# Kernel tuning notes

Hardware: AMD Instinct MI355X
Metric: run time of the kernel (lower is better)

The kernel has to match this reference:

```python
import jax, jax.numpy as jnp
from jax import lax
import numpy as np
import math

N_BLOCK = 10
CH = 64          # channels (nf)
IN_CH = 3        # input image channels
K = 3            # kernel size
COND_CH = 128    # conv_index='22' condition channel
B, H, W = 4, 128, 128


def setup_inputs() -> dict:
    key = jax.random.key(0)
    ks = jax.random.split(key, 8)
    x = jax.random.normal(ks[0], (B, IN_CH, H, W), jnp.float32)
    condition_feature = jax.random.normal(ks[1], (B, COND_CH, 1, 1), jnp.float32)
    # BaseConv2d params are torch.randn (initialize_weights skips BaseConv2d/EqualLinear)
    in_w = jax.random.normal(ks[2], (CH, IN_CH, K, K), jnp.float32)
    in_b = jnp.zeros((CH,), jnp.float32)
    blk_w = jax.random.normal(ks[3], (N_BLOCK, 2, CH, CH, K, K), jnp.float32)
    blk_b = jnp.zeros((N_BLOCK, 2, CH), jnp.float32)
    mod_w = jax.random.normal(ks[4], (N_BLOCK * 2, CH, COND_CH), jnp.float32)  # EqualLinear weights
    mod_b = jnp.ones((N_BLOCK * 2, CH), jnp.float32)                           # bias_init=1
    up_w = jax.random.normal(ks[5], (2, 4 * CH, CH, K, K), jnp.float32)        # two x2 pixel-shuffle stages
    up_b = jnp.zeros((2, 4 * CH), jnp.float32)
    out_w = jax.random.normal(ks[6], (IN_CH, CH, K, K), jnp.float32)
    out_b = jnp.zeros((IN_CH,), jnp.float32)
    return dict(x=x, condition_feature=condition_feature, in_w=in_w, in_b=in_b,
                blk_w=blk_w, blk_b=blk_b, mod_w=mod_w, mod_b=mod_b,
                up_w=up_w, up_b=up_b, out_w=out_w, out_b=out_b)


def _conv(x, w, b):
    out = lax.conv_general_dilated(x, w, (1, 1), [(K // 2, K // 2)] * 2,
                                   dimension_numbers=('NCHW', 'OIHW', 'NCHW'))
    return out + b[None, :, None, None]


def _mod_conv(x, w, bias, cond, scale):
    # x [b,c,h,w]; w [out,in,k,k]; cond [b,1,in,1,1] -> per-sample modulated weights
    wmod = w[None] * scale * cond  # [b,out,in,k,k]
    conv1 = lambda xi, wi: lax.conv_general_dilated(
        xi[None], wi, (1, 1), [(K // 2, K // 2)] * 2,
        dimension_numbers=('NCHW', 'OIHW', 'NCHW'))[0]
    out = jax.vmap(conv1)(x, wmod)  # groups=batch grouped conv
    # faithful to torch.repeat_interleave(bias, repeats=b) split across groups
    b_ = x.shape[0]
    bmat = jnp.repeat(bias, b_).reshape(b_, bias.shape[0])
    return out + bmat[:, :, None, None]


def _pixel_shuffle(x, r):
    b, c, h, w = x.shape
    C = c // (r * r)
    return x.reshape(b, C, r, r, h, w).transpose(0, 1, 4, 2, 5, 3).reshape(b, C, h * r, w * r)


def reference(x, condition_feature, in_w, in_b, blk_w, blk_b, mod_w, mod_b,
              up_w, up_b, out_w, out_b):
    b = x.shape[0]
    s_in = 1.0 / math.sqrt(IN_CH * K * K)
    s64 = 1.0 / math.sqrt(CH * K * K)
    s_lin = 1.0 / math.sqrt(COND_CH)

    # Modulations: 20 EqualLinears on [b,128] -> [10,2,b,1,64,1,1]
    cf = condition_feature.reshape(b, COND_CH)
    feats = jnp.einsum('bc,moc->mbo', cf, mod_w) * s_lin + mod_b[:, None, :]
    cond_feats = feats.reshape(N_BLOCK, 2, b, 1, CH, 1, 1)

    fea = _conv(x, in_w * s_in, in_b)
    for i in range(N_BLOCK):
        res = _mod_conv(fea, blk_w[i, 0], blk_b[i, 0], cond_feats[i, 0], s64)
        res = jax.nn.relu(res)
        res = _mod_conv(res, blk_w[i, 1], blk_b[i, 1], cond_feats[i, 1], s64)
        fea = res + fea  # residual_lr = 1
    for j in range(2):  # scale=4 -> two (conv, PixelShuffle(2)) stages
        fea = _conv(fea, up_w[j] * s64, up_b[j])
        fea = _pixel_shuffle(fea, 2)
    out = _conv(fea, out_w * s64, out_b)
    return out
```

## Files before the change

kernel.cpp:

```cpp
#include <hip/hip_runtime.h>
#include <math.h>

typedef unsigned short u16;
typedef unsigned int u32;
typedef float f32x4 __attribute__((ext_vector_type(4)));
typedef _Float16 f16;
typedef f16 f16x8 __attribute__((ext_vector_type(8)));
typedef f16 f16x4 __attribute__((ext_vector_type(4)));
typedef u32 u32x4 __attribute__((ext_vector_type(4)));


__device__ u16  g_bufT[(size_t)4*128*128*64];
__device__ float g_bufR[(size_t)4*128*128*64];
__device__ u16  g_bufB[(size_t)4*128*128*64];
__device__ u16  g_bufC[(size_t)4*4*256*256*16];
__device__ u16  g_bufE[(size_t)4*4*512*512*16];
__device__ float g_mod[20*4*64];
__device__ f16 g_wblk[(size_t)20*4*36864];
__device__ f16 g_wup[(size_t)2*4*36864];
__device__ f16 g_wout[9216];
__device__ u16 g_zero[8];

__device__ __forceinline__ void gll16(const void* g, void* l) {
    __builtin_amdgcn_global_load_lds(
        (const __attribute__((address_space(1))) unsigned*)g,
        (__attribute__((address_space(3))) unsigned*)l, 16, 0, 0);
}

__global__ void mod_kernel(const float* __restrict__ cf,
                           const float* __restrict__ mw,
                           const float* __restrict__ mb,
                           float* __restrict__ mod) {
    int m = blockIdx.x, b = blockIdx.y, o = threadIdx.x;
    const float* wrow = mw + (m * 64 + o) * 128;
    const float* cfb  = cf + b * 128;
    float s = 0.f;
#pragma unroll 8
    for (int c = 0; c < 128; ++c) s = fmaf(cfb[c], wrow[c], s);
    mod[(m * 4 + b) * 64 + o] = s * 0.08838834764831845f + mb[m * 64 + o];
}

__global__ void prep_blk_kernel(const float* __restrict__ bw,
                                const float* __restrict__ mod,
                                f16* __restrict__ wp) {
    int c = blockIdx.x, b = blockIdx.y;
    const float s64 = 1.0f / 24.0f;
    size_t base = (size_t)(c * 4 + b) * 36864;
    for (int idx = threadIdx.x; idx < 36864; idx += 256) {
        int j = idx & 7, l = (idx >> 3) & 63;
        int frag = idx >> 9;
        int mt = frag & 3, kfr = frag >> 2;
        int kf = kfr & 1, tap = kfr >> 1;
        int oc = mt * 16 + (l & 15);
        int ic = kf * 32 + (l >> 4) * 8 + j;
        float val = bw[((size_t)(c * 64 + oc) * 64 + ic) * 9 + tap] * s64 *
                    mod[(c * 4 + b) * 64 + ic];
        wp[base + idx] = (f16)val;
    }
}

__global__ void prep_up_kernel(const float* __restrict__ uw, f16* __restrict__ wp) {
    int st = blockIdx.x, ocg = blockIdx.y;
    const float s64 = 1.0f / 24.0f;
    size_t base = (size_t)(st * 4 + ocg) * 36864;
    for (int idx = threadIdx.x; idx < 36864; idx += 256) {
        int j = idx & 7, l = (idx >> 3) & 63;
        int frag = idx >> 9;
        int mt = frag & 3, kfr = frag >> 2;
        int kf = kfr & 1, tap = kfr >> 1;
        int oc = ocg * 64 + mt * 16 + (l & 15);
        int ic = kf * 32 + (l >> 4) * 8 + j;
        wp[base + idx] = (f16)(uw[((size_t)(st * 256 + oc) * 64 + ic) * 9 + tap] * s64);
    }
}

__global__ void prep_out_kernel(const float* __restrict__ ow, f16* __restrict__ wp) {
    const float s64 = 1.0f / 24.0f;
    for (int idx = threadIdx.x; idx < 9216; idx += 256) {
        int j = idx & 7, l = (idx >> 3) & 63;
        int frag = idx >> 9;
        int kf = frag & 1, tap = frag >> 1;
        int oc = l & 15;
        int ic = kf * 32 + (l >> 4) * 8 + j;
        float val = (oc < 3) ? ow[((size_t)(oc * 64) + ic) * 9 + tap] * s64 : 0.f;
        wp[idx] = (f16)val;
    }
}

__global__ __launch_bounds__(256) void in_conv_kernel(
    const float* __restrict__ in, const float* __restrict__ wgt,
    const float* __restrict__ bias, float* __restrict__ outR,
    u16* __restrict__ outT) {
    __shared__ float slds[3][34][35];
    __shared__ float wlds[3 * 9 * 16];
    const int H = 128, W = 128;
    const int tid = threadIdx.x, x = tid & 31, yb = tid >> 5;
    const int b = blockIdx.z >> 2, ocb = (blockIdx.z & 3) * 16;
    const int tY = blockIdx.y * 32, tX = blockIdx.x * 32;
    const float s_in = 0.19245008972987526f;

    float acc[16][4];
#pragma unroll
    for (int oc = 0; oc < 16; ++oc)
#pragma unroll
        for (int k = 0; k < 4; ++k) acc[oc][k] = 0.f;

    for (int idx = tid; idx < 3 * 34 * 34; idx += 256) {
        int ic = idx / (34 * 34), p = idx % (34 * 34);
        int r = p / 34, c = p % 34;
        int gy = tY + r - 1, gx = tX + c - 1;
        float v = 0.f;
        if (gy >= 0 && gy < H && gx >= 0 && gx < W)
            v = in[((b * 3 + ic) * H + gy) * W + gx] * s_in;
        slds[ic][r][c] = v;
    }
    for (int idx = tid; idx < 3 * 9 * 16; idx += 256) {
        int oc = idx & 15, tap = (idx >> 4) % 9, ic = idx / 144;
        wlds[idx] = wgt[((ocb + oc) * 3 + ic) * 9 + tap];
    }
    __syncthreads();

#pragma unroll
    for (int ic = 0; ic < 3; ++ic)
#pragma unroll
        for (int dy = 0; dy < 3; ++dy)
#pragma unroll
            for (int dx = 0; dx < 3; ++dx) {
                float xv[4];
#pragma unroll
                for (int k = 0; k < 4; ++k)
                    xv[k] = slds[ic][yb + 8 * k + dy][x + dx];
                const float* wrow = &wlds[(ic * 9 + dy * 3 + dx) * 16];
#pragma unroll
                for (int oc = 0; oc < 16; ++oc) {
                    float wv = wrow[oc];
#pragma unroll
                    for (int k = 0; k < 4; ++k) acc[oc][k] = fmaf(wv, xv[k], acc[oc][k]);
                }
            }

#pragma unroll
    for (int oc = 0; oc < 16; ++oc) {
        int goc = ocb + oc;
        float bv = bias[goc];
#pragma unroll
        for (int k = 0; k < 4; ++k) {
            int gy = tY + yb + 8 * k, gx = tX + x;
            size_t pixG = ((size_t)b * H + gy) * W + gx;
            float v = acc[oc][k] + bv;
            outR[pixG * 64 + goc] = v;
            outT[pixG * 64 + goc] = __builtin_bit_cast(u16, (f16)v);
        }
    }
}

template <int CG, int RG, int MG, int MT, int ROWS, int INMODE, int OUTMODE, int LB>
__global__ __launch_bounds__(256, LB) void mconv(
    const u16* __restrict__ inh, const f16* __restrict__ wp,
    const float* __restrict__ bias, float* __restrict__ rbuf,
    void* __restrict__ outv, u16* __restrict__ outT,
    int H, int W, int OCG, int wp_bstride, size_t in_pl, size_t out_pl)
{
    constexpr int TC = CG * 16, TR = RG * ROWS;
    constexpr int CST = TC + 2, RST = TR + 2;
    constexpr int PXT = RST * CST;
    constexpr int PXP = (PXT + 63) & ~63;
    constexpr int MT_W = MT / MG;
    constexpr int NW = CG * RG * MG;
    constexpr int SB_H = 4 * PXP * 8;
    constexpr int SA_H = 2 * 3 * MT * 512;

    __shared__ __align__(16) u16 smem[SB_H + SA_H];
    u16* sB = smem;
    u16* sA = smem + SB_H;

    const int tid = threadIdx.x;
    const int lane = tid & 63, wv = tid >> 6;
    const int lcol = lane & 15, lk8 = lane >> 4;
    const int cg = (CG > 1) ? (wv % CG) : 0;
    const int rg = (wv / CG) % RG;
    const int mg = wv / (CG * RG);
    const int b = blockIdx.z / OCG, ocg = blockIdx.z % OCG;
    const int y0 = blockIdx.y * TR, x0 = blockIdx.x * TC;
    const f16* wpb = wp + (size_t)b * wp_bstride + (size_t)ocg * 36864;

    auto stageA = [&](int kf, int dx, int buf) {
        for (int f = wv; f < 3 * MT; f += NW) {
            int dy = f / MT, mt = f - dy * MT;
            const f16* src = wpb + ((size_t)((dy * 3 + dx) * 2 + kf) * MT + mt) * 512 + lane * 8;
            gll16(src, sA + ((size_t)(buf * 3 * MT + f)) * 512 + lane * 8);
        }
    };
    auto stageB = [&](int kf) {
        for (int g0 = wv * 64; g0 < 4 * PXP; g0 += NW * 64) {
            int g = g0 + lane;
            int pl = g / PXP, px = g - pl * PXP;
            int t = px / CST, c = px - t * CST;
            int gy = y0 + t - 1, gx = x0 + c - 1;
            const void* src = g_zero;
            if (px < PXT && gy >= 0 && gy < H && gx >= 0 && gx < W) {
                size_t pix = ((size_t)b * H + gy) * W + gx;
                int ic = kf * 32 + pl * 8;
                if (INMODE == 1)
                    src = inh + pix * 64 + ic;
                else
                    src = inh + (size_t)(ic >> 4) * in_pl + pix * 16 + (ic & 15);
            }
            gll16(src, sB + (size_t)g * 8);
        }
    };

    f32x4 acc[ROWS][MT_W];
#pragma unroll
    for (int r = 0; r < ROWS; ++r)
#pragma unroll
        for (int m = 0; m < MT_W; ++m) acc[r][m] = (f32x4)0.f;

    stageB(0);
    stageA(0, 0, 0);
    __syncthreads();

    for (int s = 0; s < 6; ++s) {
        int kf = s / 3, dx = s - kf * 3;
        if (s == 3) {
            stageB(1);
            __syncthreads();
        }
        if (s < 5) {
            int ns = s + 1;
            stageA(ns / 3, ns % 3, ns & 1);
        }
        f16x8 Af[3][MT_W];
        const int abase = (s & 1) * 3 * MT;
#pragma unroll
        for (int dy = 0; dy < 3; ++dy)
#pragma unroll
            for (int m = 0; m < MT_W; ++m)
                Af[dy][m] = *(const f16x8*)(sA + (size_t)(abase + dy * MT + mg * MT_W + m) * 512 + lane * 8);

        const u16* bbase = sB + (size_t)lk8 * PXP * 8;
        const int pcol = cg * 16 + dx + lcol;
#pragma unroll
        for (int iy = 0; iy < ROWS + 2; ++iy) {
            int px = (rg * ROWS + iy) * CST + pcol;
            f16x8 Bf = *(const f16x8*)(bbase + (size_t)px * 8);
#pragma unroll
            for (int dy = 0; dy < 3; ++dy) {
                constexpr int unused = 0; (void)unused;
                int r = iy - dy;
                if (r >= 0 && r < ROWS) {
#pragma unroll
                    for (int m = 0; m < MT_W; ++m)
                        acc[r][m] = __builtin_amdgcn_mfma_f32_16x16x32_f16(
                            Af[dy][m], Bf, acc[r][m], 0, 0, 0);
                }
            }
        }
        __syncthreads();
    }

    if (OUTMODE == 0 || OUTMODE == 1) {
        u16* outh = (u16*)outv;
#pragma unroll
        for (int r = 0; r < ROWS; ++r) {
            int gy = y0 + rg * ROWS + r, gx = x0 + cg * 16 + lcol;
            size_t pixG = ((size_t)b * H + gy) * W + gx;
#pragma unroll
            for (int m = 0; m < MT_W; ++m) {
                int oc0 = (mg * MT_W + m) * 16 + lk8 * 4;
                f32x4 v = acc[r][m] + *(const f32x4*)(bias + oc0);
                if (OUTMODE == 0) {
                    f16x4 o;
#pragma unroll
                    for (int j = 0; j < 4; ++j) o[j] = (f16)fmaxf(v[j], 0.f);
                    *(f16x4*)(outh + pixG * 64 + oc0) = o;
                } else {
                    float* rp = rbuf + pixG * 64 + oc0;
                    f32x4 rv = *(const f32x4*)rp;
                    v += rv;
                    *(f32x4*)rp = v;
                    f16x4 o;
#pragma unroll
                    for (int j = 0; j < 4; ++j) o[j] = (f16)v[j];
                    *(f16x4*)(outT + pixG * 64 + oc0) = o;
                }
            }
        }
    } else if (OUTMODE == 2) {
        constexpr int NP = 2 * TR * TC;
        __syncthreads();
        u32* sT = (u32*)smem;
#pragma unroll
        for (int r = 0; r < ROWS; ++r) {
#pragma unroll
            for (int m = 0; m < MT_W; ++m) {
                int oc0 = m * 16 + lk8 * 4;
                int cc = m * 4 + lk8;
                f32x4 v = acc[r][m] + *(const f32x4*)(bias + ocg * 64 + oc0);
                int oy = 2 * (rg * ROWS + r);
#pragma unroll
                for (int jp = 0; jp < 2; ++jp) {
                    f16 e0 = (f16)v[jp * 2], e1 = (f16)v[jp * 2 + 1];
                    u32 w = (u32)__builtin_bit_cast(u16, e0) |
                            ((u32)__builtin_bit_cast(u16, e1) << 16);
                    sT[cc * NP + (oy + jp) * TC + cg * 16 + lcol] = w;
                }
            }
        }
        __syncthreads();
        u16* outh = (u16*)outv + (size_t)ocg * out_pl;
        const int H2 = 2 * H, W2 = 2 * W;
#pragma unroll
        for (int it = 0; it < NP / 256; ++it) {
            int p = tid + it * 256;
            int oy = p / TC, xp = p - oy * TC;
            u32 tv[16];
#pragma unroll
            for (int c = 0; c < 16; ++c) tv[c] = sT[c * NP + p];
            u32 q0[8], q1[8];
#pragma unroll
            for (int c2 = 0; c2 < 8; ++c2) {
                q0[c2] = (tv[2 * c2] & 0xffffu) | (tv[2 * c2 + 1] << 16);
                q1[c2] = (tv[2 * c2] >> 16) | (tv[2 * c2 + 1] & 0xffff0000u);
            }
            int gy2 = 2 * y0 + oy, gx2 = 2 * x0 + 2 * xp;
            u16* dst = outh + (((size_t)b * H2 + gy2) * W2 + gx2) * 16;
            *(u32x4*)(dst)      = *(u32x4*)(q0);
            *(u32x4*)(dst + 8)  = *(u32x4*)(q0 + 4);
            *(u32x4*)(dst + 16) = *(u32x4*)(q1);
            *(u32x4*)(dst + 24) = *(u32x4*)(q1 + 4);
        }
    } else {
        float* outp = (float*)outv;
        if (lk8 == 0) {
#pragma unroll
            for (int r = 0; r < ROWS; ++r) {
                int gy = y0 + rg * ROWS + r, gx = x0 + cg * 16 + lcol;
#pragma unroll
                for (int j = 0; j < 3; ++j) {
                    float v = acc[r][0][j] + bias[j];
                    outp[(((size_t)b * 3 + j) * H + gy) * W + gx] = v;
                }
            }
        }
    }
}

extern "C" void kernel_launch(void* const* d_in, const int* in_sizes, int n_in,
                              void* d_out, int out_size, void* d_ws, size_t ws_size,
                              hipStream_t stream) {
    const float* x     = (const float*)d_in[0];
    const float* cf    = (const float*)d_in[1];
    const float* in_w  = (const float*)d_in[2];
    const float* in_b  = (const float*)d_in[3];
    const float* blk_w = (const float*)d_in[4];
    const float* blk_b = (const float*)d_in[5];
    const float* mod_w = (const float*)d_in[6];
    const float* mod_b = (const float*)d_in[7];
    const float* up_w  = (const float*)d_in[8];
    const float* up_b  = (const float*)d_in[9];
    const float* out_w = (const float*)d_in[10];
    const float* out_b = (const float*)d_in[11];
    float* outp = (float*)d_out;

    u16 *bufT, *bufB, *bufC, *bufE;
    float *bufR, *modp;
    f16 *wblk, *wup, *wout;
    hipGetSymbolAddress((void**)&bufT, HIP_SYMBOL(g_bufT));
    hipGetSymbolAddress((void**)&bufR, HIP_SYMBOL(g_bufR));
    hipGetSymbolAddress((void**)&bufB, HIP_SYMBOL(g_bufB));
    hipGetSymbolAddress((void**)&bufC, HIP_SYMBOL(g_bufC));
    hipGetSymbolAddress((void**)&bufE, HIP_SYMBOL(g_bufE));
    hipGetSymbolAddress((void**)&modp, HIP_SYMBOL(g_mod));
    hipGetSymbolAddress((void**)&wblk, HIP_SYMBOL(g_wblk));
    hipGetSymbolAddress((void**)&wup,  HIP_SYMBOL(g_wup));
    hipGetSymbolAddress((void**)&wout, HIP_SYMBOL(g_wout));

    mod_kernel<<<dim3(20, 4), 64, 0, stream>>>(cf, mod_w, mod_b, modp);
    prep_blk_kernel<<<dim3(20, 4), 256, 0, stream>>>(blk_w, modp, wblk);
    prep_up_kernel<<<dim3(2, 4), 256, 0, stream>>>(up_w, wup);
    prep_out_kernel<<<1, 256, 0, stream>>>(out_w, wout);

    in_conv_kernel<<<dim3(4, 4, 16), 256, 0, stream>>>(x, in_w, in_b, bufR, bufT);

    const size_t PLC = (size_t)4 * 256 * 256 * 16;
    const size_t PLE = (size_t)4 * 512 * 512 * 16;

    for (int i = 0; i < 10; ++i) {
        mconv<1, 2, 2, 4, 4, 1, 0, 2><<<dim3(8, 16, 4), 256, 0, stream>>>(
            bufT, wblk + (size_t)(2 * i) * 4 * 36864, blk_b + (2 * i) * 64,
            nullptr, bufB, nullptr, 128, 128, 1, 36864, 0, 0);
        mconv<1, 2, 2, 4, 4, 1, 1, 2><<<dim3(8, 16, 4), 256, 0, stream>>>(
            bufB, wblk + (size_t)(2 * i + 1) * 4 * 36864, blk_b + (2 * i + 1) * 64,
            bufR, nullptr, bufT, 128, 128, 1, 36864, 0, 0);
    }

    mconv<2, 2, 1, 4, 8, 1, 2, 2><<<dim3(4, 8, 16), 256, 0, stream>>>(
        bufT, wup, up_b, nullptr, bufC, nullptr, 128, 128, 4, 0, 0, PLC);
    mconv<2, 2, 1, 4, 8, 2, 2, 2><<<dim3(8, 16, 16), 256, 0, stream>>>(
        bufC, wup + (size_t)4 * 36864, up_b + 256, nullptr, bufE, nullptr,
        256, 256, 4, 0, PLC, PLE);
    mconv<2, 2, 1, 1, 8, 2, 3, 3><<<dim3(16, 32, 4), 256, 0, stream>>>(
        bufE, wout, out_b, nullptr, outp, nullptr, 512, 512, 1, 0, PLE, 0);
}
```

Before: 540.1 us.

## Load weights directly to registers and stage all input channels once

```diff
diff --git a/kernel.cpp b/kernel.cpp
--- a/kernel.cpp
+++ b/kernel.cpp
@@ -155,7 +155,7 @@
 }
 
 template <int CG, int RG, int MG, int MT, int ROWS, int INMODE, int OUTMODE, int LB>
-__global__ __launch_bounds__(256, LB) void mconv(
+__global__ __launch_bounds__(CG* RG* MG * 64, LB) void mconv(
     const u16* __restrict__ inh, const f16* __restrict__ wp,
     const float* __restrict__ bias, float* __restrict__ rbuf,
     void* __restrict__ outv, u16* __restrict__ outT,
@@ -164,15 +164,14 @@
     constexpr int TC = CG * 16, TR = RG * ROWS;
     constexpr int CST = TC + 2, RST = TR + 2;
     constexpr int PXT = RST * CST;
-    constexpr int PXP = (PXT + 63) & ~63;
     constexpr int MT_W = MT / MG;
     constexpr int NW = CG * RG * MG;
-    constexpr int SB_H = 4 * PXP * 8;
-    constexpr int SA_H = 2 * 3 * MT * 512;
-
-    __shared__ __align__(16) u16 smem[SB_H + SA_H];
-    u16* sB = smem;
-    u16* sA = smem + SB_H;
+    constexpr int NTHR = NW * 64;
+    constexpr int SB_H = 8 * PXT * 8;
+    constexpr int NP = 2 * TR * TC;
+    constexpr int SMEM_H = (OUTMODE == 2 && 16 * NP * 2 > SB_H) ? 16 * NP * 2 : SB_H;
+
+    __shared__ __align__(16) u16 smem[SMEM_H];
 
     const int tid = threadIdx.x;
     const int lane = tid & 63, wv = tid >> 6;
@@ -184,31 +183,36 @@
     const int y0 = blockIdx.y * TR, x0 = blockIdx.x * TC;
     const f16* wpb = wp + (size_t)b * wp_bstride + (size_t)ocg * 36864;
 
-    auto stageA = [&](int kf, int dx, int buf) {
-        for (int f = wv; f < 3 * MT; f += NW) {
-            int dy = f / MT, mt = f - dy * MT;
-            const f16* src = wpb + ((size_t)((dy * 3 + dx) * 2 + kf) * MT + mt) * 512 + lane * 8;
-            gll16(src, sA + ((size_t)(buf * 3 * MT + f)) * 512 + lane * 8);
-        }
+    auto loadA = [&](int s, f16x8(&A)[3][MT_W]) {
+        int kf = s / 3, dx = s - kf * 3;
+#pragma unroll
+        for (int dy = 0; dy < 3; ++dy)
+#pragma unroll
+            for (int m = 0; m < MT_W; ++m) {
+                int frag = ((dy * 3 + dx) * 2 + kf) * MT + mg * MT_W + m;
+                A[dy][m] = *(const f16x8*)(wpb + (size_t)frag * 512 + (size_t)lane * 8);
+            }
     };
-    auto stageB = [&](int kf) {
-        for (int g0 = wv * 64; g0 < 4 * PXP; g0 += NW * 64) {
-            int g = g0 + lane;
-            int pl = g / PXP, px = g - pl * PXP;
-            int t = px / CST, c = px - t * CST;
-            int gy = y0 + t - 1, gx = x0 + c - 1;
-            const void* src = g_zero;
-            if (px < PXT && gy >= 0 && gy < H && gx >= 0 && gx < W) {
-                size_t pix = ((size_t)b * H + gy) * W + gx;
-                int ic = kf * 32 + pl * 8;
-                if (INMODE == 1)
-                    src = inh + pix * 64 + ic;
-                else
-                    src = inh + (size_t)(ic >> 4) * in_pl + pix * 16 + (ic & 15);
-            }
-            gll16(src, sB + (size_t)g * 8);
-        }
-    };
+
+    f16x8 Ab[2][3][MT_W];
+    loadA(0, Ab[0]);
+
+    for (int g = tid; g < 8 * PXT; g += NTHR) {
+        int pl = g / PXT, px = g - pl * PXT;
+        int t = px / CST, c = px - t * CST;
+        int gy = y0 + t - 1, gx = x0 + c - 1;
+        const void* src = g_zero;
+        if (gy >= 0 && gy < H && gx >= 0 && gx < W) {
+            size_t pix = ((size_t)b * H + gy) * W + gx;
+            int ic = pl * 8;
+            if (INMODE == 1)
+                src = inh + pix * 64 + ic;
+            else
+                src = inh + (size_t)(ic >> 4) * in_pl + pix * 16 + (ic & 15);
+        }
+        gll16(src, smem + (size_t)g * 8);
+    }
+    __syncthreads();
 
     f32x4 acc[ROWS][MT_W];
 #pragma unroll
@@ -216,47 +220,27 @@
 #pragma unroll
         for (int m = 0; m < MT_W; ++m) acc[r][m] = (f32x4)0.f;
 
-    stageB(0);
-    stageA(0, 0, 0);
-    __syncthreads();
-
+#pragma unroll
     for (int s = 0; s < 6; ++s) {
-        int kf = s / 3, dx = s - kf * 3;
-        if (s == 3) {
-            stageB(1);
-            __syncthreads();
-        }
-        if (s < 5) {
-            int ns = s + 1;
-            stageA(ns / 3, ns % 3, ns & 1);
-        }
-        f16x8 Af[3][MT_W];
-        const int abase = (s & 1) * 3 * MT;
-#pragma unroll
-        for (int dy = 0; dy < 3; ++dy)
-#pragma unroll
-            for (int m = 0; m < MT_W; ++m)
-                Af[dy][m] = *(const f16x8*)(sA + (size_t)(abase + dy * MT + mg * MT_W + m) * 512 + lane * 8);
-
-        const u16* bbase = sB + (size_t)lk8 * PXP * 8;
+        if (s < 5) loadA(s + 1, Ab[(s + 1) & 1]);
+        const int kf = s / 3, dx = s - kf * 3;
+        const u16* bp = smem + (size_t)(kf * 4 + lk8) * PXT * 8;
         const int pcol = cg * 16 + dx + lcol;
 #pragma unroll
         for (int iy = 0; iy < ROWS + 2; ++iy) {
             int px = (rg * ROWS + iy) * CST + pcol;
-            f16x8 Bf = *(const f16x8*)(bbase + (size_t)px * 8);
+            f16x8 Bf = *(const f16x8*)(bp + (size_t)px * 8);
 #pragma unroll
             for (int dy = 0; dy < 3; ++dy) {
-                constexpr int unused = 0; (void)unused;
                 int r = iy - dy;
                 if (r >= 0 && r < ROWS) {
 #pragma unroll
                     for (int m = 0; m < MT_W; ++m)
                         acc[r][m] = __builtin_amdgcn_mfma_f32_16x16x32_f16(
-                            Af[dy][m], Bf, acc[r][m], 0, 0, 0);
-                }
-            }
-        }
-        __syncthreads();
+                            Ab[s & 1][dy][m], Bf, acc[r][m], 0, 0, 0);
+                }
+            }
+        }
     }
 
     if (OUTMODE == 0 || OUTMODE == 1) {
@@ -287,15 +271,14 @@
             }
         }
     } else if (OUTMODE == 2) {
-        constexpr int NP = 2 * TR * TC;
         __syncthreads();
         u32* sT = (u32*)smem;
 #pragma unroll
         for (int r = 0; r < ROWS; ++r) {
 #pragma unroll
             for (int m = 0; m < MT_W; ++m) {
-                int oc0 = m * 16 + lk8 * 4;
-                int cc = m * 4 + lk8;
+                int oc0 = (mg * MT_W + m) * 16 + lk8 * 4;
+                int cc = (mg * MT_W + m) * 4 + lk8;
                 f32x4 v = acc[r][m] + *(const f32x4*)(bias + ocg * 64 + oc0);
                 int oy = 2 * (rg * ROWS + r);
 #pragma unroll
@@ -311,8 +294,8 @@
         u16* outh = (u16*)outv + (size_t)ocg * out_pl;
         const int H2 = 2 * H, W2 = 2 * W;
 #pragma unroll
-        for (int it = 0; it < NP / 256; ++it) {
-            int p = tid + it * 256;
+        for (int it = 0; it < NP / NTHR; ++it) {
+            int p = tid + it * NTHR;
             int oy = p / TC, xp = p - oy * TC;
             u32 tv[16];
 #pragma unroll
@@ -387,19 +370,19 @@
     const size_t PLE = (size_t)4 * 512 * 512 * 16;
 
     for (int i = 0; i < 10; ++i) {
-        mconv<1, 2, 2, 4, 4, 1, 0, 2><<<dim3(8, 16, 4), 256, 0, stream>>>(
+        mconv<1, 2, 2, 4, 4, 1, 0, 3><<<dim3(8, 16, 4), 256, 0, stream>>>(
             bufT, wblk + (size_t)(2 * i) * 4 * 36864, blk_b + (2 * i) * 64,
             nullptr, bufB, nullptr, 128, 128, 1, 36864, 0, 0);
-        mconv<1, 2, 2, 4, 4, 1, 1, 2><<<dim3(8, 16, 4), 256, 0, stream>>>(
+        mconv<1, 2, 2, 4, 4, 1, 1, 3><<<dim3(8, 16, 4), 256, 0, stream>>>(
             bufB, wblk + (size_t)(2 * i + 1) * 4 * 36864, blk_b + (2 * i + 1) * 64,
             bufR, nullptr, bufT, 128, 128, 1, 36864, 0, 0);
     }
 
-    mconv<2, 2, 1, 4, 8, 1, 2, 2><<<dim3(4, 8, 16), 256, 0, stream>>>(
+    mconv<2, 1, 2, 4, 8, 1, 2, 3><<<dim3(4, 16, 16), 256, 0, stream>>>(
         bufT, wup, up_b, nullptr, bufC, nullptr, 128, 128, 4, 0, 0, PLC);
-    mconv<2, 2, 1, 4, 8, 2, 2, 2><<<dim3(8, 16, 16), 256, 0, stream>>>(
+    mconv<2, 1, 2, 4, 8, 2, 2, 3><<<dim3(8, 32, 16), 256, 0, stream>>>(
         bufC, wup + (size_t)4 * 36864, up_b + 256, nullptr, bufE, nullptr,
         256, 256, 4, 0, PLC, PLE);
-    mconv<2, 2, 1, 1, 8, 2, 3, 3><<<dim3(16, 32, 4), 256, 0, stream>>>(
+    mconv<2, 2, 1, 1, 4, 2, 3, 4><<<dim3(16, 64, 4), 256, 0, stream>>>(
         bufE, wout, out_b, nullptr, outp, nullptr, 512, 512, 1, 0, PLE, 0);
 }
```

Measured after the change: 543.7 us. No clear change (+0.7%).
